# Performance work log

Hardware: AMD Instinct MI355X
Metric: run time of the kernel (lower is better)

The kernel has to match this reference:

```python
import jax, jax.numpy as jnp
import numpy as np

NEG_INF = -1e30


def setup_inputs() -> dict:
    key = jax.random.key(0)
    k1, k2, k3, k4, k5, k6 = jax.random.split(key, 6)
    B, CL, QL, H = 16, 512, 64, 768
    c = jax.random.normal(k1, (B, CL, H), dtype=jnp.float32)
    q = jax.random.normal(k2, (B, QL, H), dtype=jnp.float32)
    c_mask = jax.random.randint(k3, (B, CL), 0, 2, dtype=jnp.int32)
    q_mask = jax.random.randint(k4, (B, QL), 0, 2, dtype=jnp.int32)
    W = jax.random.normal(k5, (H, H), dtype=jnp.float32) * (1.0 / np.sqrt(H))
    b = jax.random.normal(k6, (H,), dtype=jnp.float32) * 0.01
    return {"c": c, "q": q, "c_mask": c_mask, "q_mask": q_mask, "W": W, "b": b}


def reference(c, q, c_mask, q_mask, W, b):
    # c: [B, CL, H], q: [B, QL, H]
    cm = c_mask.astype(bool)[:, :, None]   # [B, CL, 1]
    qm = q_mask.astype(bool)[:, None, :]   # [B, 1, QL]
    # projected context then similarity matrix s: [B, CL, QL]
    cp = jnp.einsum('bch,dh->bcd', c, W) + b
    s = jnp.einsum('bcd,bqd->bcq', cp, q)
    # dual masked softmax (c2q over query dim, q2c over context dim)
    s1 = jax.nn.softmax(jnp.where(qm, s, NEG_INF), axis=2)  # [B, CL, QL]
    s2 = jax.nn.softmax(jnp.where(cm, s, NEG_INF), axis=1)  # [B, CL, QL]
    # a = s1 @ q : context-to-query attention
    a = jnp.einsum('bcq,bqh->bch', s1, q)
    # bvec = (s1 @ s2^T) @ c : query-to-context attention
    ss = jnp.einsum('bcq,bdq->bcd', s1, s2)  # [B, CL, CL]
    bvec = jnp.einsum('bcd,bdh->bch', ss, c)
    x = jnp.concatenate([c, a, c * a, c * bvec], axis=2)  # [B, CL, 4H]
    return x
```

## Files before the change

### kernel.cpp

```cpp
#include <hip/hip_runtime.h>
#include <math.h>


#define B_  16
#define CL_ 512
#define QL_ 64
#define H_  768
#define M_  (B_ * CL_)

typedef __attribute__((ext_vector_type(8))) short s8v;
typedef __attribute__((ext_vector_type(4))) float f4v;

__device__ __forceinline__ unsigned short bf16_rne(float x) {
    unsigned int u = __float_as_uint(x);
    u += 0x7fffu + ((u >> 16) & 1u);
    return (unsigned short)(u >> 16);
}
__device__ __forceinline__ float bf16_f(unsigned short h) {
    return __uint_as_float((unsigned int)h << 16);
}
__device__ __forceinline__ void split2(float x, unsigned short& h, unsigned short& l) {
    h = bf16_rne(x);
    l = bf16_rne(x - bf16_f(h));
}

__global__ __launch_bounds__(256) void k_u_beta(const float* __restrict__ q,
    const float* __restrict__ W, const float* __restrict__ bias,
    unsigned short* __restrict__ uh, unsigned short* __restrict__ ul,
    float* __restrict__ beta)
{
    if (blockIdx.x >= 192) {
        const int row = (blockIdx.x - 192) * 4 + (threadIdx.x >> 6);
        const int lane = threadIdx.x & 63;
        float p = 0.f;
        for (int d = lane; d < H_; d += 64) p = fmaf(bias[d], q[(size_t)row * H_ + d], p);
#pragma unroll
        for (int o = 32; o; o >>= 1) p += __shfl_xor(p, o);
        if (lane == 0) beta[row] = p;
        return;
    }
    __shared__ unsigned short Wh[64][40], Wl[64][40];
    const int m0 = (blockIdx.x & 15) * 64, n0 = (blockIdx.x >> 4) * 64;
    const int t = threadIdx.x, w = t >> 6, lane = t & 63;
    const int fm = lane & 15, quad = lane >> 4;
    const int mrow = m0 + w * 16 + fm;
    const int dd = t >> 3, hc = (t & 7) * 8;
    f4v acc[4];
#pragma unroll
    for (int j = 0; j < 4; ++j) acc[j] = (f4v){0.f, 0.f, 0.f, 0.f};
    for (int k0 = 0; k0 < H_; k0 += 32) {
        const float* wp = &W[(size_t)(k0 + dd) * H_ + n0 + hc];
        const float4 v0 = *(const float4*)wp, v1 = *(const float4*)(wp + 4);
        const float* ap = &q[(size_t)mrow * H_ + k0 + quad * 8];
        const float4 a0 = *(const float4*)ap, a1 = *(const float4*)(ap + 4);
        const float as[8] = {a0.x, a0.y, a0.z, a0.w, a1.x, a1.y, a1.z, a1.w};
        s8v fah, fal;
#pragma unroll
        for (int j = 0; j < 8; ++j) { unsigned short h, l; split2(as[j], h, l); fah[j] = (short)h; fal[j] = (short)l; }
        const float ws[8] = {v0.x, v0.y, v0.z, v0.w, v1.x, v1.y, v1.z, v1.w};
        __syncthreads();
#pragma unroll
        for (int j = 0; j < 8; ++j) {
            unsigned short h, l; split2(ws[j], h, l);
            Wh[hc + j][dd] = h; Wl[hc + j][dd] = l;
        }
        __syncthreads();
#pragma unroll
        for (int tn = 0; tn < 4; ++tn) {
            const s8v bh = *(const s8v*)&Wh[tn * 16 + fm][quad * 8];
            const s8v bl = *(const s8v*)&Wl[tn * 16 + fm][quad * 8];
            acc[tn] = __builtin_amdgcn_mfma_f32_16x16x32_bf16(fah, bh, acc[tn], 0, 0, 0);
            acc[tn] = __builtin_amdgcn_mfma_f32_16x16x32_bf16(fah, bl, acc[tn], 0, 0, 0);
            acc[tn] = __builtin_amdgcn_mfma_f32_16x16x32_bf16(fal, bh, acc[tn], 0, 0, 0);
        }
    }
#pragma unroll
    for (int tn = 0; tn < 4; ++tn) {
        const int col = n0 + tn * 16 + fm;
#pragma unroll
        for (int r = 0; r < 4; ++r) {
            const int row = m0 + w * 16 + quad * 4 + r;
            unsigned short h, l; split2(acc[tn][r], h, l);
            uh[(size_t)row * H_ + col] = h;
            ul[(size_t)row * H_ + col] = l;
        }
    }
}

__global__ __launch_bounds__(256) void k_s_sm(const float* __restrict__ c,
    const unsigned short* __restrict__ uh, const unsigned short* __restrict__ ul,
    const float* __restrict__ beta, const int* __restrict__ q_mask,
    float* __restrict__ sT, unsigned short* __restrict__ s1)
{
    __shared__ unsigned short chh[2][16][40], cll[2][16][40];
    __shared__ float sL[16][65];
    const int m0 = blockIdx.x * 16;
    const int batch = m0 >> 9;
    const int cloc = m0 & (CL_ - 1);
    const int t = threadIdx.x, w = t >> 6, lane = t & 63;
    const int fm = lane & 15, quad = lane >> 4;
    const int srow = t >> 4, skk = (t & 15) * 2;
    f4v acc = (f4v){0.f, 0.f, 0.f, 0.f};

    float2 v = *(const float2*)&c[(size_t)(m0 + srow) * H_ + skk];
    int p = 0;
    for (int k0 = 0; k0 < H_; k0 += 32) {
        unsigned short h0s, l0s, h1s, l1s;
        split2(v.x, h0s, l0s); split2(v.y, h1s, l1s);
        *(ushort2*)&chh[p][srow][skk] = make_ushort2(h0s, h1s);
        *(ushort2*)&cll[p][srow][skk] = make_ushort2(l0s, l1s);
        __syncthreads();
        if (k0 + 32 < H_) v = *(const float2*)&c[(size_t)(m0 + srow) * H_ + k0 + 32 + skk];
        const s8v fah = *(const s8v*)&chh[p][fm][quad * 8];
        const s8v fal = *(const s8v*)&cll[p][fm][quad * 8];
        const size_t bo = (size_t)(batch * QL_ + w * 16 + fm) * H_ + k0 + quad * 8;
        const s8v bh = *(const s8v*)&uh[bo];
        const s8v bl = *(const s8v*)&ul[bo];
        acc = __builtin_amdgcn_mfma_f32_16x16x32_bf16(fah, bh, acc, 0, 0, 0);
        acc = __builtin_amdgcn_mfma_f32_16x16x32_bf16(fah, bl, acc, 0, 0, 0);
        acc = __builtin_amdgcn_mfma_f32_16x16x32_bf16(fal, bh, acc, 0, 0, 0);
        p ^= 1;
    }
    {
        const int col = w * 16 + fm;
        const float bb = beta[batch * QL_ + col];
#pragma unroll
        for (int r = 0; r < 4; ++r) {
            const int lr = quad * 4 + r;
            sL[lr][col] = acc[r] + bb;
        }
    }
    __syncthreads();
    const bool qm = q_mask[batch * QL_ + lane] != 0;
#pragma unroll
    for (int rr = 0; rr < 4; ++rr) {
        const int lr = w * 4 + rr;
        const float x = qm ? sL[lr][lane] : -1e30f;
        float mx = x;
#pragma unroll
        for (int o = 32; o; o >>= 1) mx = fmaxf(mx, __shfl_xor(mx, o));
        const float e = __expf(x - mx);
        float sm = e;
#pragma unroll
        for (int o = 32; o; o >>= 1) sm += __shfl_xor(sm, o);
        s1[(size_t)(m0 + lr) * QL_ + lane] = bf16_rne(e / sm);
    }
    {
        const int qq = t >> 2, c4o = (t & 3) * 4;
        float4 ov;
        ov.x = sL[c4o + 0][qq];
        ov.y = sL[c4o + 1][qq];
        ov.z = sL[c4o + 2][qq];
        ov.w = sL[c4o + 3][qq];
        *(float4*)&sT[((size_t)batch * QL_ + qq) * CL_ + cloc + c4o] = ov;
    }
}

__global__ __launch_bounds__(256) void k_tfin3(const float* __restrict__ sT,
    const unsigned short* __restrict__ s1, const float* __restrict__ q,
    const float* __restrict__ c, const int* __restrict__ c_mask,
    float* __restrict__ out)
{
    __shared__ unsigned short s2L[64 * 512];
    __shared__ unsigned short qT[64][72];
    __shared__ unsigned short tT[64][72];
    __shared__ unsigned short Bs[2][64][40];
    const int h0 = blockIdx.x * 64;
    const int b  = blockIdx.y;
    const int t = threadIdx.x, w = t >> 6, lane = t & 63;
    const int fm = lane & 15, quad = lane >> 4;

    {
        const int cbase8 = lane * 8;
        int cm8[8];
#pragma unroll
        for (int j = 0; j < 8; ++j) cm8[j] = c_mask[b * CL_ + cbase8 + j];
        const float* stb = sT + (size_t)b * QL_ * CL_;
        for (int qi = 0; qi < 16; ++qi) {
            const int qq = w * 16 + qi;
            const float* sr = stb + (size_t)qq * CL_ + cbase8;
            const float4 v0 = *(const float4*)sr, v1 = *(const float4*)(sr + 4);
            float x[8] = {v0.x, v0.y, v0.z, v0.w, v1.x, v1.y, v1.z, v1.w};
#pragma unroll
            for (int j = 0; j < 8; ++j) x[j] = cm8[j] ? x[j] : -1e30f;
            float m = x[0];
#pragma unroll
            for (int j = 1; j < 8; ++j) m = fmaxf(m, x[j]);
#pragma unroll
            for (int o = 32; o; o >>= 1) m = fmaxf(m, __shfl_xor(m, o));
            float e[8], sm = 0.f;
#pragma unroll
            for (int j = 0; j < 8; ++j) { e[j] = __expf(x[j] - m); sm += e[j]; }
#pragma unroll
            for (int o = 32; o; o >>= 1) sm += __shfl_xor(sm, o);
            const float inv = 1.f / sm;
            s8v sv;
#pragma unroll
            for (int j = 0; j < 8; ++j) sv[j] = (short)bf16_rne(e[j] * inv);
            const int boff = ((qq * 512 + cbase8) * 2) ^ ((qq & 7) << 4);
            *(s8v*)((char*)s2L + boff) = sv;
        }
    }

    {
        const int r = t >> 4, c4 = (t & 15) * 4;
#pragma unroll
        for (int i = 0; i < 4; ++i) {
            const int qr = r + 16 * i;
            const float4 v = *(const float4*)&q[((size_t)b * QL_ + qr) * H_ + h0 + c4];
            qT[c4 + 0][qr] = bf16_rne(v.x);
            qT[c4 + 1][qr] = bf16_rne(v.y);
            qT[c4 + 2][qr] = bf16_rne(v.z);
            qT[c4 + 3][qr] = bf16_rne(v.w);
        }
    }

    {
        const int dd = t >> 3, hc = (t & 7) * 8;
        f4v acc[4];
#pragma unroll
        for (int j = 0; j < 4; ++j) acc[j] = (f4v){0.f, 0.f, 0.f, 0.f};
        const float* cp0 = &c[((size_t)b * CL_ + dd) * H_ + h0 + hc];
        float4 v0 = *(const float4*)cp0, v1 = *(const float4*)(cp0 + 4);
        int p = 0;
        for (int d0 = 0; d0 < CL_; d0 += 32) {
            const float xs[8] = {v0.x, v0.y, v0.z, v0.w, v1.x, v1.y, v1.z, v1.w};
#pragma unroll
            for (int j = 0; j < 8; ++j) Bs[p][hc + j][dd] = bf16_rne(xs[j]);
            __syncthreads();
            if (d0 + 32 < CL_) {
                const float* cp = &c[((size_t)b * CL_ + d0 + 32 + dd) * H_ + h0 + hc];
                v0 = *(const float4*)cp; v1 = *(const float4*)(cp + 4);
            }
            const s8v fb = *(const s8v*)&Bs[p][w * 16 + fm][quad * 8];
#pragma unroll
            for (int tm = 0; tm < 4; ++tm) {
                const int boff = (((tm * 16 + fm) * 512 + d0 + quad * 8) * 2) ^ ((fm & 7) << 4);
                const s8v fa = *(const s8v*)((const char*)s2L + boff);
                acc[tm] = __builtin_amdgcn_mfma_f32_16x16x32_bf16(fa, fb, acc[tm], 0, 0, 0);
            }
            p ^= 1;
        }
#pragma unroll
        for (int tm = 0; tm < 4; ++tm)
#pragma unroll
            for (int r = 0; r < 4; ++r)
                tT[w * 16 + fm][tm * 16 + quad * 4 + r] = bf16_rne(acc[tm][r]);
    }
    __syncthreads();

    for (int cc = 0; cc < 2; ++cc) {
        const int cbase = cc * 256 + w * 64;
        f4v aa[4][4], bb[4][4];
#pragma unroll
        for (int i = 0; i < 4; ++i)
#pragma unroll
            for (int j = 0; j < 4; ++j) { aa[i][j] = (f4v){0.f, 0.f, 0.f, 0.f}; bb[i][j] = aa[i][j]; }
#pragma unroll
        for (int ks = 0; ks < 2; ++ks) {
            s8v fa[4], fq[4], ft[4];
#pragma unroll
            for (int tm = 0; tm < 4; ++tm)
                fa[tm] = *(const s8v*)&s1[(size_t)(b * CL_ + cbase + tm * 16 + fm) * QL_ + ks * 32 + quad * 8];
#pragma unroll
            for (int tn = 0; tn < 4; ++tn) {
                fq[tn] = *(const s8v*)&qT[tn * 16 + fm][ks * 32 + quad * 8];
                ft[tn] = *(const s8v*)&tT[tn * 16 + fm][ks * 32 + quad * 8];
            }
#pragma unroll
            for (int tm = 0; tm < 4; ++tm)
#pragma unroll
                for (int tn = 0; tn < 4; ++tn) {
                    aa[tm][tn] = __builtin_amdgcn_mfma_f32_16x16x32_bf16(fa[tm], fq[tn], aa[tm][tn], 0, 0, 0);
                    bb[tm][tn] = __builtin_amdgcn_mfma_f32_16x16x32_bf16(fa[tm], ft[tn], bb[tm][tn], 0, 0, 0);
                }
        }
#pragma unroll
        for (int tm = 0; tm < 4; ++tm)
#pragma unroll
            for (int tn = 0; tn < 4; ++tn) {
                const int h = h0 + tn * 16 + fm;
#pragma unroll
                for (int r = 0; r < 4; ++r) {
                    const int crow = cbase + tm * 16 + quad * 4 + r;
                    const float cv = c[((size_t)b * CL_ + crow) * H_ + h];
                    const float av = aa[tm][tn][r], bv = bb[tm][tn][r];
                    float* ob = out + (size_t)(b * CL_ + crow) * (4 * H_);
                    ob[h]           = cv;
                    ob[H_ + h]      = av;
                    ob[2 * H_ + h]  = cv * av;
                    ob[3 * H_ + h]  = cv * bv;
                }
            }
    }
}

extern "C" void kernel_launch(void* const* d_in, const int* in_sizes, int n_in,
                              void* d_out, int out_size, void* d_ws, size_t ws_size,
                              hipStream_t stream) {
    const float* c      = (const float*)d_in[0];
    const float* q      = (const float*)d_in[1];
    const int*   c_mask = (const int*)d_in[2];
    const int*   q_mask = (const int*)d_in[3];
    const float* W      = (const float*)d_in[4];
    const float* bias   = (const float*)d_in[5];
    float* out = (float*)d_out;

    char* base = (char*)d_ws;
    unsigned short* uh   = (unsigned short*)(base);
    unsigned short* ul   = (unsigned short*)(base + 1572864);
    float*          beta = (float*)(base + 3145728);
    float*          sT   = (float*)(base + 3149824);
    unsigned short* s1   = (unsigned short*)(base + 5246976);

    dim3 blk(256);
    k_u_beta <<<dim3(192 + 256),  blk, 0, stream>>>(q, W, bias, uh, ul, beta);
    k_s_sm   <<<dim3(512),        blk, 0, stream>>>(c, uh, ul, beta, q_mask, sT, s1);
    k_tfin3  <<<dim3(12, 16),     blk, 0, stream>>>(sT, s1, q, c, c_mask, out);
}
```

Before: 207.5 us.

## Split q2c softmax into partial stats and double the final kernel grid

k_s_sm now writes per-16-row partial max/sum statistics for the context-dim softmax and pre-masks sT. k_tfin3 merges these partials instead of recomputing the full softmax, and rebuilds s2 fragments on the fly from sT with exp. This drops the 64 KB s2 LDS buffer, which should raise occupancy. The grid also doubles by splitting the context rows into halves, at the cost of the (S1@T) T-matrix stage being recomputed by both halves. Register prefetch of the next k-slice is added in k_u_beta and k_s_sm to overlap global loads with MFMA work.

Result: slower. 214.2 us (+3.2%).

```diff
diff --git a/kernel.cpp b/kernel.cpp
--- a/kernel.cpp
+++ b/kernel.cpp
@@ -48,21 +48,27 @@
     f4v acc[4];
 #pragma unroll
     for (int j = 0; j < 4; ++j) acc[j] = (f4v){0.f, 0.f, 0.f, 0.f};
+    const float* wp0 = &W[(size_t)dd * H_ + n0 + hc];
+    float4 v0 = *(const float4*)wp0, v1 = *(const float4*)(wp0 + 4);
+    const float* ap0 = &q[(size_t)mrow * H_ + quad * 8];
+    float4 a0 = *(const float4*)ap0, a1 = *(const float4*)(ap0 + 4);
     for (int k0 = 0; k0 < H_; k0 += 32) {
-        const float* wp = &W[(size_t)(k0 + dd) * H_ + n0 + hc];
-        const float4 v0 = *(const float4*)wp, v1 = *(const float4*)(wp + 4);
-        const float* ap = &q[(size_t)mrow * H_ + k0 + quad * 8];
-        const float4 a0 = *(const float4*)ap, a1 = *(const float4*)(ap + 4);
         const float as[8] = {a0.x, a0.y, a0.z, a0.w, a1.x, a1.y, a1.z, a1.w};
         s8v fah, fal;
 #pragma unroll
         for (int j = 0; j < 8; ++j) { unsigned short h, l; split2(as[j], h, l); fah[j] = (short)h; fal[j] = (short)l; }
-        const float ws[8] = {v0.x, v0.y, v0.z, v0.w, v1.x, v1.y, v1.z, v1.w};
+        const float ws_[8] = {v0.x, v0.y, v0.z, v0.w, v1.x, v1.y, v1.z, v1.w};
         __syncthreads();
 #pragma unroll
         for (int j = 0; j < 8; ++j) {
-            unsigned short h, l; split2(ws[j], h, l);
+            unsigned short h, l; split2(ws_[j], h, l);
             Wh[hc + j][dd] = h; Wl[hc + j][dd] = l;
+        }
+        if (k0 + 32 < H_) {
+            const float* wp = &W[(size_t)(k0 + 32 + dd) * H_ + n0 + hc];
+            v0 = *(const float4*)wp; v1 = *(const float4*)(wp + 4);
+            const float* ap = &q[(size_t)mrow * H_ + k0 + 32 + quad * 8];
+            a0 = *(const float4*)ap; a1 = *(const float4*)(ap + 4);
         }
         __syncthreads();
 #pragma unroll
@@ -90,7 +96,9 @@
 __global__ __launch_bounds__(256) void k_s_sm(const float* __restrict__ c,
     const unsigned short* __restrict__ uh, const unsigned short* __restrict__ ul,
     const float* __restrict__ beta, const int* __restrict__ q_mask,
-    float* __restrict__ sT, unsigned short* __restrict__ s1)
+    const int* __restrict__ c_mask,
+    float* __restrict__ sT, unsigned short* __restrict__ s1,
+    float* __restrict__ pstats)
 {
     __shared__ unsigned short chh[2][16][40], cll[2][16][40];
     __shared__ float sL[16][65];
@@ -102,6 +110,10 @@
     const int srow = t >> 4, skk = (t & 15) * 2;
     f4v acc = (f4v){0.f, 0.f, 0.f, 0.f};
 
+    const size_t bo0 = (size_t)(batch * QL_ + w * 16 + fm) * H_ + quad * 8;
+    s8v bh = *(const s8v*)&uh[bo0];
+    s8v bl = *(const s8v*)&ul[bo0];
+
     float2 v = *(const float2*)&c[(size_t)(m0 + srow) * H_ + skk];
     int p = 0;
     for (int k0 = 0; k0 < H_; k0 += 32) {
@@ -111,14 +123,17 @@
         *(ushort2*)&cll[p][srow][skk] = make_ushort2(l0s, l1s);
         __syncthreads();
         if (k0 + 32 < H_) v = *(const float2*)&c[(size_t)(m0 + srow) * H_ + k0 + 32 + skk];
+        s8v nbh = bh, nbl = bl;
+        if (k0 + 32 < H_) {
+            nbh = *(const s8v*)&uh[bo0 + k0 + 32];
+            nbl = *(const s8v*)&ul[bo0 + k0 + 32];
+        }
         const s8v fah = *(const s8v*)&chh[p][fm][quad * 8];
         const s8v fal = *(const s8v*)&cll[p][fm][quad * 8];
-        const size_t bo = (size_t)(batch * QL_ + w * 16 + fm) * H_ + k0 + quad * 8;
-        const s8v bh = *(const s8v*)&uh[bo];
-        const s8v bl = *(const s8v*)&ul[bo];
         acc = __builtin_amdgcn_mfma_f32_16x16x32_bf16(fah, bh, acc, 0, 0, 0);
         acc = __builtin_amdgcn_mfma_f32_16x16x32_bf16(fah, bl, acc, 0, 0, 0);
         acc = __builtin_amdgcn_mfma_f32_16x16x32_bf16(fal, bh, acc, 0, 0, 0);
+        bh = nbh; bl = nbl;
         p ^= 1;
     }
     {
@@ -145,60 +160,70 @@
         for (int o = 32; o; o >>= 1) sm += __shfl_xor(sm, o);
         s1[(size_t)(m0 + lr) * QL_ + lane] = bf16_rne(e / sm);
     }
+    if (w == 0) {
+        float xs[16];
+        float pm = -1e30f;
+#pragma unroll
+        for (int r = 0; r < 16; ++r) {
+            const float xv = c_mask[batch * CL_ + cloc + r] ? sL[r][lane] : -1e30f;
+            xs[r] = xv; pm = fmaxf(pm, xv);
+        }
+        float ps = 0.f;
+#pragma unroll
+        for (int r = 0; r < 16; ++r) ps += __expf(xs[r] - pm);
+        const int tile = cloc >> 4;
+        *(float2*)&pstats[((size_t)(batch * 32 + tile) * 64 + lane) * 2] = make_float2(pm, ps);
+    }
     {
         const int qq = t >> 2, c4o = (t & 3) * 4;
+        const int cb = batch * CL_ + cloc + c4o;
         float4 ov;
-        ov.x = sL[c4o + 0][qq];
-        ov.y = sL[c4o + 1][qq];
-        ov.z = sL[c4o + 2][qq];
-        ov.w = sL[c4o + 3][qq];
+        ov.x = c_mask[cb + 0] ? sL[c4o + 0][qq] : -1e30f;
+        ov.y = c_mask[cb + 1] ? sL[c4o + 1][qq] : -1e30f;
+        ov.z = c_mask[cb + 2] ? sL[c4o + 2][qq] : -1e30f;
+        ov.w = c_mask[cb + 3] ? sL[c4o + 3][qq] : -1e30f;
         *(float4*)&sT[((size_t)batch * QL_ + qq) * CL_ + cloc + c4o] = ov;
     }
 }
 
 __global__ __launch_bounds__(256) void k_tfin3(const float* __restrict__ sT,
+    const float* __restrict__ pstats,
     const unsigned short* __restrict__ s1, const float* __restrict__ q,
-    const float* __restrict__ c, const int* __restrict__ c_mask,
-    float* __restrict__ out)
+    const float* __restrict__ c, float* __restrict__ out)
 {
-    __shared__ unsigned short s2L[64 * 512];
     __shared__ unsigned short qT[64][72];
     __shared__ unsigned short tT[64][72];
     __shared__ unsigned short Bs[2][64][40];
-    const int h0 = blockIdx.x * 64;
-    const int b  = blockIdx.y;
+    __shared__ float sredm[4][64], sreds[4][64];
+    __shared__ float statsM[64], statsI[64];
+    const int h0   = blockIdx.x * 64;
+    const int b    = blockIdx.y >> 1;
+    const int half = blockIdx.y & 1;
     const int t = threadIdx.x, w = t >> 6, lane = t & 63;
     const int fm = lane & 15, quad = lane >> 4;
 
     {
-        const int cbase8 = lane * 8;
-        int cm8[8];
-#pragma unroll
-        for (int j = 0; j < 8; ++j) cm8[j] = c_mask[b * CL_ + cbase8 + j];
-        const float* stb = sT + (size_t)b * QL_ * CL_;
-        for (int qi = 0; qi < 16; ++qi) {
-            const int qq = w * 16 + qi;
-            const float* sr = stb + (size_t)qq * CL_ + cbase8;
-            const float4 v0 = *(const float4*)sr, v1 = *(const float4*)(sr + 4);
-            float x[8] = {v0.x, v0.y, v0.z, v0.w, v1.x, v1.y, v1.z, v1.w};
-#pragma unroll
-            for (int j = 0; j < 8; ++j) x[j] = cm8[j] ? x[j] : -1e30f;
-            float m = x[0];
-#pragma unroll
-            for (int j = 1; j < 8; ++j) m = fmaxf(m, x[j]);
-#pragma unroll
-            for (int o = 32; o; o >>= 1) m = fmaxf(m, __shfl_xor(m, o));
-            float e[8], sm = 0.f;
-#pragma unroll
-            for (int j = 0; j < 8; ++j) { e[j] = __expf(x[j] - m); sm += e[j]; }
-#pragma unroll
-            for (int o = 32; o; o >>= 1) sm += __shfl_xor(sm, o);
-            const float inv = 1.f / sm;
-            s8v sv;
-#pragma unroll
-            for (int j = 0; j < 8; ++j) sv[j] = (short)bf16_rne(e[j] * inv);
-            const int boff = ((qq * 512 + cbase8) * 2) ^ ((qq & 7) << 4);
-            *(s8v*)((char*)s2L + boff) = sv;
+        float2 pp[8];
+        const float* pb = pstats + (size_t)b * 32 * 64 * 2;
+#pragma unroll
+        for (int i = 0; i < 8; ++i)
+            pp[i] = *(const float2*)&pb[((size_t)(w * 8 + i) * 64 + lane) * 2];
+        float m = pp[0].x;
+#pragma unroll
+        for (int i = 1; i < 8; ++i) m = fmaxf(m, pp[i].x);
+        sredm[w][lane] = m;
+        __syncthreads();
+        m = fmaxf(fmaxf(sredm[0][lane], sredm[1][lane]),
+                  fmaxf(sredm[2][lane], sredm[3][lane]));
+        float ss = 0.f;
+#pragma unroll
+        for (int i = 0; i < 8; ++i) ss += pp[i].y * __expf(pp[i].x - m);
+        sreds[w][lane] = ss;
+        __syncthreads();
+        if (w == 0) {
+            const float sum = sreds[0][lane] + sreds[1][lane] + sreds[2][lane] + sreds[3][lane];
+            statsM[lane] = m;
+            statsI[lane] = 1.f / sum;
         }
     }
 
@@ -214,6 +239,14 @@
             qT[c4 + 3][qr] = bf16_rne(v.w);
         }
     }
+    __syncthreads();
+
+    float qm_[4], qi_[4];
+#pragma unroll
+    for (int tm = 0; tm < 4; ++tm) {
+        qm_[tm] = statsM[tm * 16 + fm];
+        qi_[tm] = statsI[tm * 16 + fm];
+    }
 
     {
         const int dd = t >> 3, hc = (t & 7) * 8;
@@ -222,8 +255,18 @@
         for (int j = 0; j < 4; ++j) acc[j] = (f4v){0.f, 0.f, 0.f, 0.f};
         const float* cp0 = &c[((size_t)b * CL_ + dd) * H_ + h0 + hc];
         float4 v0 = *(const float4*)cp0, v1 = *(const float4*)(cp0 + 4);
+        const float* sp[4];
+#pragma unroll
+        for (int tm = 0; tm < 4; ++tm)
+            sp[tm] = &sT[((size_t)b * QL_ + tm * 16 + fm) * CL_ + quad * 8];
         int p = 0;
         for (int d0 = 0; d0 < CL_; d0 += 32) {
+            float4 s0[4], s1r[4];
+#pragma unroll
+            for (int tm = 0; tm < 4; ++tm) {
+                s0[tm]  = *(const float4*)(sp[tm] + d0);
+                s1r[tm] = *(const float4*)(sp[tm] + d0 + 4);
+            }
             const float xs[8] = {v0.x, v0.y, v0.z, v0.w, v1.x, v1.y, v1.z, v1.w};
 #pragma unroll
             for (int j = 0; j < 8; ++j) Bs[p][hc + j][dd] = bf16_rne(xs[j]);
@@ -235,8 +278,12 @@
             const s8v fb = *(const s8v*)&Bs[p][w * 16 + fm][quad * 8];
 #pragma unroll
             for (int tm = 0; tm < 4; ++tm) {
-                const int boff = (((tm * 16 + fm) * 512 + d0 + quad * 8) * 2) ^ ((fm & 7) << 4);
-                const s8v fa = *(const s8v*)((const char*)s2L + boff);
+                const float ex[8] = {s0[tm].x, s0[tm].y, s0[tm].z, s0[tm].w,
+                                     s1r[tm].x, s1r[tm].y, s1r[tm].z, s1r[tm].w};
+                s8v fa;
+#pragma unroll
+                for (int j = 0; j < 8; ++j)
+                    fa[j] = (short)bf16_rne(__expf(ex[j] - qm_[tm]) * qi_[tm]);
                 acc[tm] = __builtin_amdgcn_mfma_f32_16x16x32_bf16(fa, fb, acc[tm], 0, 0, 0);
             }
             p ^= 1;
@@ -249,8 +296,8 @@
     }
     __syncthreads();
 
-    for (int cc = 0; cc < 2; ++cc) {
-        const int cbase = cc * 256 + w * 64;
+    {
+        const int cbase = half * 256 + w * 64;
         f4v aa[4][4], bb[4][4];
 #pragma unroll
         for (int i = 0; i < 4; ++i)
@@ -307,14 +354,15 @@
     float* out = (float*)d_out;
 
     char* base = (char*)d_ws;
-    unsigned short* uh   = (unsigned short*)(base);
-    unsigned short* ul   = (unsigned short*)(base + 1572864);
-    float*          beta = (float*)(base + 3145728);
-    float*          sT   = (float*)(base + 3149824);
-    unsigned short* s1   = (unsigned short*)(base + 5246976);
+    unsigned short* uh     = (unsigned short*)(base);
+    unsigned short* ul     = (unsigned short*)(base + 1572864);
+    float*          beta   = (float*)(base + 3145728);
+    float*          sT     = (float*)(base + 3149824);
+    unsigned short* s1     = (unsigned short*)(base + 5246976);
+    float*          pstats = (float*)(base + 6295552);
 
     dim3 blk(256);
     k_u_beta <<<dim3(192 + 256),  blk, 0, stream>>>(q, W, bias, uh, ul, beta);
-    k_s_sm   <<<dim3(512),        blk, 0, stream>>>(c, uh, ul, beta, q_mask, sT, s1);
-    k_tfin3  <<<dim3(12, 16),     blk, 0, stream>>>(sT, s1, q, c, c_mask, out);
-}
+    k_s_sm   <<<dim3(512),        blk, 0, stream>>>(c, uh, ul, beta, q_mask, c_mask, sT, s1, pstats);
+    k_tfin3  <<<dim3(12, 32),     blk, 0, stream>>>(sT, pstats, s1, q, c, out);
+}
```

## Double k_tfin3 block to 512 threads and split the CL reduction across two wave groups

Applied to the files above, without the earlier changes.

The final kernel now runs 512 threads per block instead of 256. The s2 softmax and q-transpose loads are spread over twice as many waves. The s2·c product over the 512 context rows is split between two groups of four waves, each reducing 256 rows, and the partial sums are combined through LDS (reusing the s2L buffer). The output stage then covers all 512 context rows in a single pass with eight waves instead of two passes with four. The goal is more parallelism and latency hiding on a grid of only 192 blocks, at the cost of extra LDS traffic, extra barriers and higher register pressure at 512 threads.

After: 197.3 us. 4.9% less time.

```diff
diff --git a/kernel.cpp b/kernel.cpp
--- a/kernel.cpp
+++ b/kernel.cpp
@@ -156,19 +156,21 @@
     }
 }
 
-__global__ __launch_bounds__(256) void k_tfin3(const float* __restrict__ sT,
+__global__ __launch_bounds__(512) void k_tfin3(const float* __restrict__ sT,
     const unsigned short* __restrict__ s1, const float* __restrict__ q,
     const float* __restrict__ c, const int* __restrict__ c_mask,
     float* __restrict__ out)
 {
     __shared__ unsigned short s2L[64 * 512];
+    __shared__ unsigned short Bs[2][2][64][40];
     __shared__ unsigned short qT[64][72];
     __shared__ unsigned short tT[64][72];
-    __shared__ unsigned short Bs[2][64][40];
     const int h0 = blockIdx.x * 64;
     const int b  = blockIdx.y;
     const int t = threadIdx.x, w = t >> 6, lane = t & 63;
     const int fm = lane & 15, quad = lane >> 4;
+    const int grp = w >> 2;
+    const int wl  = w & 3;
 
     {
         const int cbase8 = lane * 8;
@@ -176,8 +178,9 @@
 #pragma unroll
         for (int j = 0; j < 8; ++j) cm8[j] = c_mask[b * CL_ + cbase8 + j];
         const float* stb = sT + (size_t)b * QL_ * CL_;
-        for (int qi = 0; qi < 16; ++qi) {
-            const int qq = w * 16 + qi;
+#pragma unroll
+        for (int qi = 0; qi < 8; ++qi) {
+            const int qq = w * 8 + qi;
             const float* sr = stb + (size_t)qq * CL_ + cbase8;
             const float4 v0 = *(const float4*)sr, v1 = *(const float4*)(sr + 4);
             float x[8] = {v0.x, v0.y, v0.z, v0.w, v1.x, v1.y, v1.z, v1.w};
@@ -205,8 +208,8 @@
     {
         const int r = t >> 4, c4 = (t & 15) * 4;
 #pragma unroll
-        for (int i = 0; i < 4; ++i) {
-            const int qr = r + 16 * i;
+        for (int i = 0; i < 2; ++i) {
+            const int qr = r + 32 * i;
             const float4 v = *(const float4*)&q[((size_t)b * QL_ + qr) * H_ + h0 + c4];
             qT[c4 + 0][qr] = bf16_rne(v.x);
             qT[c4 + 1][qr] = bf16_rne(v.y);
@@ -215,42 +218,59 @@
         }
     }
 
-    {
-        const int dd = t >> 3, hc = (t & 7) * 8;
-        f4v acc[4];
-#pragma unroll
-        for (int j = 0; j < 4; ++j) acc[j] = (f4v){0.f, 0.f, 0.f, 0.f};
-        const float* cp0 = &c[((size_t)b * CL_ + dd) * H_ + h0 + hc];
+    f4v acc[4];
+#pragma unroll
+    for (int j = 0; j < 4; ++j) acc[j] = (f4v){0.f, 0.f, 0.f, 0.f};
+    {
+        const int tl = t & 255;
+        const int dd = tl >> 3, hc = (tl & 7) * 8;
+        const int gbase = grp * 256;
+        const float* cp0 = &c[((size_t)b * CL_ + gbase + dd) * H_ + h0 + hc];
         float4 v0 = *(const float4*)cp0, v1 = *(const float4*)(cp0 + 4);
         int p = 0;
-        for (int d0 = 0; d0 < CL_; d0 += 32) {
+        for (int d0 = 0; d0 < 256; d0 += 32) {
             const float xs[8] = {v0.x, v0.y, v0.z, v0.w, v1.x, v1.y, v1.z, v1.w};
 #pragma unroll
-            for (int j = 0; j < 8; ++j) Bs[p][hc + j][dd] = bf16_rne(xs[j]);
+            for (int j = 0; j < 8; ++j) Bs[grp][p][hc + j][dd] = bf16_rne(xs[j]);
             __syncthreads();
-            if (d0 + 32 < CL_) {
-                const float* cp = &c[((size_t)b * CL_ + d0 + 32 + dd) * H_ + h0 + hc];
+            if (d0 + 32 < 256) {
+                const float* cp = &c[((size_t)b * CL_ + gbase + d0 + 32 + dd) * H_ + h0 + hc];
                 v0 = *(const float4*)cp; v1 = *(const float4*)(cp + 4);
             }
-            const s8v fb = *(const s8v*)&Bs[p][w * 16 + fm][quad * 8];
+            const s8v fb = *(const s8v*)&Bs[grp][p][wl * 16 + fm][quad * 8];
 #pragma unroll
             for (int tm = 0; tm < 4; ++tm) {
-                const int boff = (((tm * 16 + fm) * 512 + d0 + quad * 8) * 2) ^ ((fm & 7) << 4);
+                const int boff = (((tm * 16 + fm) * 512 + gbase + d0 + quad * 8) * 2) ^ ((fm & 7) << 4);
                 const s8v fa = *(const s8v*)((const char*)s2L + boff);
                 acc[tm] = __builtin_amdgcn_mfma_f32_16x16x32_bf16(fa, fb, acc[tm], 0, 0, 0);
             }
             p ^= 1;
         }
-#pragma unroll
-        for (int tm = 0; tm < 4; ++tm)
-#pragma unroll
-            for (int r = 0; r < 4; ++r)
-                tT[w * 16 + fm][tm * 16 + quad * 4 + r] = bf16_rne(acc[tm][r]);
     }
     __syncthreads();
-
-    for (int cc = 0; cc < 2; ++cc) {
-        const int cbase = cc * 256 + w * 64;
+    {
+        float* dumpf = (float*)s2L;
+        if (grp == 1) {
+#pragma unroll
+            for (int tm = 0; tm < 4; ++tm)
+#pragma unroll
+                for (int r = 0; r < 4; ++r)
+                    dumpf[((wl * 4 + tm) * 4 + r) * 64 + lane] = acc[tm][r];
+        }
+        __syncthreads();
+        if (grp == 0) {
+#pragma unroll
+            for (int tm = 0; tm < 4; ++tm)
+#pragma unroll
+                for (int r = 0; r < 4; ++r)
+                    tT[wl * 16 + fm][tm * 16 + quad * 4 + r] =
+                        bf16_rne(acc[tm][r] + dumpf[((wl * 4 + tm) * 4 + r) * 64 + lane]);
+        }
+    }
+    __syncthreads();
+
+    {
+        const int cbase = w * 64;
         f4v aa[4][4], bb[4][4];
 #pragma unroll
         for (int i = 0; i < 4; ++i)
@@ -313,8 +333,7 @@
     float*          sT   = (float*)(base + 3149824);
     unsigned short* s1   = (unsigned short*)(base + 5246976);
 
-    dim3 blk(256);
-    k_u_beta <<<dim3(192 + 256),  blk, 0, stream>>>(q, W, bias, uh, ul, beta);
-    k_s_sm   <<<dim3(512),        blk, 0, stream>>>(c, uh, ul, beta, q_mask, sT, s1);
-    k_tfin3  <<<dim3(12, 16),     blk, 0, stream>>>(sT, s1, q, c, c_mask, out);
-}
+    k_u_beta <<<dim3(192 + 256), dim3(256), 0, stream>>>(q, W, bias, uh, ul, beta);
+    k_s_sm   <<<dim3(512),       dim3(256), 0, stream>>>(c, uh, ul, beta, q_mask, sT, s1);
+    k_tfin3  <<<dim3(12, 16),    dim3(512), 0, stream>>>(sT, s1, q, c, c_mask, out);
+}
```
